# Performance work log

Hardware: AMD Instinct MI355X
Metric: run time of the kernel (lower is better)

Reference implementation:

```python
import jax, jax.numpy as jnp
import numpy as np

NUM_HEADS = 16


def setup_inputs() -> dict:
    key = jax.random.key(0)
    ks = jax.random.split(key, 4)
    B, C, T, D = 1, 1, 3072, 1024
    s = 1.0 / np.sqrt(D)
    return {
        "x": jax.random.normal(ks[0], (B, C, T, D), dtype=jnp.float32),
        "Wq": jax.random.normal(ks[1], (D, D), dtype=jnp.float32) * s,
        "bq": jnp.zeros((D,), dtype=jnp.float32),
        "Wk": jax.random.normal(ks[2], (D, D), dtype=jnp.float32) * s,
        "bk": jnp.zeros((D,), dtype=jnp.float32),
        "Wv": jax.random.normal(ks[3], (D, D), dtype=jnp.float32) * s,
        "bv": jnp.zeros((D,), dtype=jnp.float32),
        "gamma": jnp.float32(0.5),  # learned scalar; 0.0 at torch init, nonzero here for a meaningful signal
    }


def reference(x, Wq, bq, Wk, bk, Wv, bv, gamma):
    # x: (B, C, T, D); Linear acts on last dim (torch: y = x @ W.T + b)
    B, C, T, D = x.shape
    H = NUM_HEADS
    q = (jnp.einsum("bctd,ed->bcte", x, Wq) + bq).reshape(B, -1, T, H)  # (B, X, T, H), X = C*D/H
    k = (jnp.einsum("bctd,ed->bcte", x, Wk) + bk).reshape(B, -1, T, H)
    v = (jnp.einsum("bctd,ed->bcte", x, Wv) + bv).reshape(B, -1, T, H)
    q = q.transpose(0, 3, 2, 1)  # (B, H, T, X)
    k = k.transpose(0, 3, 1, 2)  # (B, H, X, T)
    energy = q @ k               # (B, H, T, T)  -- note: NO 1/sqrt(d) scaling, as in source
    attn = jax.nn.softmax(energy, axis=-1)
    v = v.transpose(0, 3, 2, 1)  # (B, H, T, X)
    out = attn @ v               # (B, H, T, X)
    out = out.transpose(0, 2, 3, 1).reshape(B, T, -1)  # (B, T, X*H) = (B, T, C*D)
    # residual broadcast: (B, T, C*D) + (B, C, T, D); valid since B == C == 1
    return gamma * out + x
```

## Files before the change

### kernel.cpp

```cpp
#include <hip/hip_runtime.h>


typedef _Float16 v8h __attribute__((ext_vector_type(8)));
typedef _Float16 v4h __attribute__((ext_vector_type(4)));
typedef __fp16   v2pk __attribute__((ext_vector_type(2)));
typedef __fp16   v4pk __attribute__((ext_vector_type(4)));
typedef float    v4f __attribute__((ext_vector_type(4)));

#define TSEQ 3072
#define DM   1024
#define NH   16
#define XD   64
#define LOG2E 1.44269504f

__device__ __forceinline__ void async_load16(const void* g, void* l) {
  __builtin_amdgcn_global_load_lds(
      (const __attribute__((address_space(1))) unsigned int*)g,
      (__attribute__((address_space(3))) unsigned int*)l,
      16, 0, 0);
}

__device__ __forceinline__ float fexp2(float x) {
  float r; asm("v_exp_f32 %0, %1" : "=v"(r) : "v"(x)); return r;
}
__device__ __forceinline__ float flog2(float x) {
  float r; asm("v_log_f32 %0, %1" : "=v"(r) : "v"(x)); return r;
}

extern "C" __global__ __launch_bounds__(256) void cvt_kernel(
    const float* __restrict__ x, const float* __restrict__ wq,
    const float* __restrict__ wk, const float* __restrict__ wv,
    _Float16* __restrict__ xb, _Float16* __restrict__ wb)
{
  const int NX4 = (TSEQ * DM) / 4;
  const int NT  = NX4 * 2;
  for (int i = blockIdx.x * blockDim.x + threadIdx.x; i < NT;
       i += gridDim.x * blockDim.x) {
    float4 v;
    _Float16* dst;
    if (i < NX4) {
      v = ((const float4*)x)[i];
      dst = xb + (size_t)i * 4;
    } else {
      const int j = i - NX4;
      const int n = j >> 8;
      if (n < 1024)      v = ((const float4*)wq)[j];
      else if (n < 2048) v = ((const float4*)wk)[j - 262144];
      else               v = ((const float4*)wv)[j - 524288];
      dst = wb + (size_t)j * 4;
    }
    v4h h;
    h[0] = (_Float16)v.x; h[1] = (_Float16)v.y;
    h[2] = (_Float16)v.z; h[3] = (_Float16)v.w;
    *(v4h*)dst = h;
  }
}

extern "C" __global__ __launch_bounds__(256) void qkv_gemm_kernel(
    const _Float16* __restrict__ xb, const _Float16* __restrict__ wb,
    const float* __restrict__ bq, const float* __restrict__ bk,
    const float* __restrict__ bv,
    _Float16* __restrict__ qlin, _Float16* __restrict__ klin,
    _Float16* __restrict__ vlin)
{
  __shared__ _Float16 As[128 * 32];
  __shared__ _Float16 Bs[128 * 32];
  const int tid = threadIdx.x;
  const int w = tid >> 6, l = tid & 63;
  const int li = l & 15, lg = l >> 4;
  const int wm = w >> 1, wn = w & 1;
  const int bid = blockIdx.x;
  const int swz = (bid & 7) * 72 + (bid >> 3);
  const int m0 = (swz / 24) * 128, n0 = (swz % 24) * 128;
  v4f acc[4][4] = {};
  const int srow = l >> 2;
  const int scol = (l & 3) * 8;
  for (int k0 = 0; k0 < DM; k0 += 32) {
#pragma unroll
    for (int c = 0; c < 2; ++c) {
      const int rbase = c * 64 + w * 16;
      async_load16(xb + (size_t)(m0 + rbase + srow) * DM + k0 + scol, &As[rbase * 32]);
      async_load16(wb + (size_t)(n0 + rbase + srow) * DM + k0 + scol, &Bs[rbase * 32]);
    }
    __syncthreads();
    v8h af[4], bf[4];
#pragma unroll
    for (int mi = 0; mi < 4; ++mi)
      af[mi] = *(const v8h*)&As[(wm * 64 + mi * 16 + li) * 32 + lg * 8];
#pragma unroll
    for (int ni = 0; ni < 4; ++ni)
      bf[ni] = *(const v8h*)&Bs[(wn * 64 + ni * 16 + li) * 32 + lg * 8];
#pragma unroll
    for (int mi = 0; mi < 4; ++mi)
#pragma unroll
      for (int ni = 0; ni < 4; ++ni)
        acc[mi][ni] = __builtin_amdgcn_mfma_f32_16x16x32_f16(
            af[mi], bf[ni], acc[mi][ni], 0, 0, 0);
    __syncthreads();
  }
  const int which = n0 >> 10;
  const int ebase = n0 & 1023;
  const float* bias = which == 0 ? bq : (which == 1 ? bk : bv);
  _Float16* outp = which == 0 ? qlin : (which == 1 ? klin : vlin);
#pragma unroll
  for (int mi = 0; mi < 4; ++mi)
#pragma unroll
    for (int r = 0; r < 4; ++r) {
      const int t = m0 + wm * 64 + mi * 16 + lg * 4 + r;
#pragma unroll
      for (int ni = 0; ni < 4; ++ni) {
        const int e = ebase + wn * 64 + ni * 16 + li;
        outp[(size_t)t * DM + e] = (_Float16)(acc[mi][ni][r] + bias[e]);
      }
    }
}

extern "C" __global__ __launch_bounds__(256) void repack_kernel(
    const _Float16* __restrict__ qlin, const _Float16* __restrict__ klin,
    const _Float16* __restrict__ vlin,
    _Float16* __restrict__ qh, _Float16* __restrict__ kh,
    _Float16* __restrict__ vt)
{
  const int NE = NH * TSEQ * XD;
  for (int g = blockIdx.x * blockDim.x + threadIdx.x; g < 3 * NE;
       g += gridDim.x * blockDim.x) {
    if (g < 2 * NE) {
      const int gg = (g < NE) ? g : g - NE;
      const int xx = gg & 63;
      const int rest = gg >> 6;
      const int h = rest / TSEQ;
      const int i = rest - h * TSEQ;
      const int t = xx * 48 + (i >> 6);
      const int e = ((i & 63) << 4) + h;
      if (g < NE) qh[gg] = qlin[t * DM + e];
      else        kh[gg] = (_Float16)((float)klin[t * DM + e] * LOG2E);
    } else {
      const int o = g - 2 * NE;
      const int j = o % TSEQ;
      const int rest = o / TSEQ;
      const int xx = rest & 63;
      const int h = rest >> 6;
      const int t = xx * 48 + (j >> 6);
      const int e = ((j & 63) << 4) + h;
      vt[o] = vlin[t * DM + e];
    }
  }
}

extern "C" __global__ __launch_bounds__(512, 2) void attn_kernel(
    const _Float16* __restrict__ qh, const _Float16* __restrict__ kh,
    const _Float16* __restrict__ vt, _Float16* __restrict__ pOut)
{
  __shared__ _Float16 SH[16384];
  __shared__ float sml[192];
  const int tid = threadIdx.x;
  const int w = tid >> 6, l = tid & 63;
  const int li = l & 15, lg = l >> 4;
  const int rw = w & 3, g = w >> 2;
  const int b = blockIdx.x;
  const int idx = b >> 3;
  const int head = (b & 7) + ((idx >= 16) ? 8 : 0);
  const int i0 = (idx & 15) * 192;
  const size_t hb = (size_t)head * TSEQ * XD;

  v8h qf[3][2];
#pragma unroll
  for (int ct = 0; ct < 3; ++ct) {
    const _Float16* qrow = qh + hb + (size_t)(i0 + rw * 48 + ct * 16 + li) * XD;
    qf[ct][0] = *(const v8h*)(qrow + lg * 8);
    qf[ct][1] = *(const v8h*)(qrow + 32 + lg * 8);
  }
  float m2[3] = {24.0f * LOG2E, 24.0f * LOG2E, 24.0f * LOG2E};
  float l4[3] = {0.0f, 0.0f, 0.0f};
  v4f oacc[4][3] = {};
  const int r8 = l >> 3, c8 = l & 7;

  for (int j0 = 0; j0 < TSEQ; j0 += 128) {
    const int jt = j0 + g * 64;
#pragma unroll
    for (int s = 0; s < 2; ++s) {
      const int n = rw * 2 + s;
      const int row = n * 8 + r8;
      async_load16(kh + hb + (size_t)(jt + row) * XD + ((c8 ^ (row & 7)) * 8),
                   &SH[g * 4096 + n * 512]);
      async_load16(vt + hb + (size_t)row * TSEQ + jt + ((c8 ^ (row & 7)) * 8),
                   &SH[8192 + g * 4096 + n * 512]);
    }
    __syncthreads();
    const _Float16* Kc = &SH[g * 4096];
    const _Float16* Vc = &SH[8192 + g * 4096];

    v4f e4[3][4];
#pragma unroll
    for (int kt = 0; kt < 4; ++kt) {
      const int krow = kt * 16 + li;
      const v8h kf0 = *(const v8h*)&Kc[krow * 64 + ((lg ^ (li & 7)) * 8)];
      const v8h kf1 = *(const v8h*)&Kc[krow * 64 + (((4 + lg) ^ (li & 7)) * 8)];
#pragma unroll
      for (int ct = 0; ct < 3; ++ct) {
        v4f a = {-m2[ct], -m2[ct], -m2[ct], -m2[ct]};
        a = __builtin_amdgcn_mfma_f32_16x16x32_f16(kf0, qf[ct][0], a, 0, 0, 0);
        a = __builtin_amdgcn_mfma_f32_16x16x32_f16(kf1, qf[ct][1], a, 0, 0, 0);
        e4[ct][kt] = a;
      }
    }

    float gm = -1.0e30f;
#pragma unroll
    for (int ct = 0; ct < 3; ++ct)
#pragma unroll
      for (int kt = 0; kt < 4; ++kt)
        gm = fmaxf(fmaxf(gm, fmaxf(e4[ct][kt][0], e4[ct][kt][1])),
                   fmaxf(e4[ct][kt][2], e4[ct][kt][3]));
    if (__any(gm > 11.5f)) {
#pragma unroll
      for (int ct = 0; ct < 3; ++ct) {
        float rm = -1.0e30f;
#pragma unroll
        for (int kt = 0; kt < 4; ++kt)
          rm = fmaxf(fmaxf(rm, fmaxf(e4[ct][kt][0], e4[ct][kt][1])),
                     fmaxf(e4[ct][kt][2], e4[ct][kt][3]));
        rm = fmaxf(rm, __shfl_xor(rm, 16, 64));
        rm = fmaxf(rm, __shfl_xor(rm, 32, 64));
        rm = fmaxf(rm, 0.0f);
        const float fs = fexp2(-rm);
#pragma unroll
        for (int kt = 0; kt < 4; ++kt)
#pragma unroll
          for (int r = 0; r < 4; ++r) e4[ct][kt][r] -= rm;
        l4[ct] *= fs;
#pragma unroll
        for (int mi = 0; mi < 4; ++mi) oacc[mi][ct] *= fs;
        m2[ct] += rm;
      }
    }

    v4h pv[3][4];
#pragma unroll
    for (int ct = 0; ct < 3; ++ct) {
#pragma unroll
      for (int kt = 0; kt < 4; ++kt) {
        const float p0 = fexp2(e4[ct][kt][0]);
        const float p1 = fexp2(e4[ct][kt][1]);
        const float p2 = fexp2(e4[ct][kt][2]);
        const float p3 = fexp2(e4[ct][kt][3]);
        const v2pk lo = __builtin_amdgcn_cvt_pkrtz(p0, p1);
        const v2pk hi = __builtin_amdgcn_cvt_pkrtz(p2, p3);
        const v4pk pk = __builtin_shufflevector(lo, hi, 0, 1, 2, 3);
        pv[ct][kt] = __builtin_bit_cast(v4h, pk);
        l4[ct] += (p0 + p1) + (p2 + p3);
      }
    }

#pragma unroll
    for (int mi = 0; mi < 4; ++mi) {
      const int vrow = mi * 16 + li;
      const int vb = vrow * 64 + (lg & 1) * 4;
#pragma unroll
      for (int kt = 0; kt < 4; ++kt) {
        const v4h vf = *(const v4h*)&Vc[vb + (((kt * 2 + (lg >> 1)) ^ (li & 7)) * 8)];
#pragma unroll
        for (int ct = 0; ct < 3; ++ct)
          oacc[mi][ct] = __builtin_amdgcn_mfma_f32_16x16x16f16(
              vf, pv[ct][kt], oacc[mi][ct], 0, 0, 0);
      }
    }
    __syncthreads();
  }

  float sv[3], inv[3];
#pragma unroll
  for (int ct = 0; ct < 3; ++ct) {
    float ls = l4[ct];
    ls += __shfl_xor(ls, 16, 64);
    ls += __shfl_xor(ls, 32, 64);
    inv[ct] = 1.0f / ls;
    sv[ct] = m2[ct] + flog2(ls);
  }
  _Float16* mb = &SH[0];
  if (g == 1) {
#pragma unroll
    for (int ct = 0; ct < 3; ++ct) {
      const int rl = rw * 48 + ct * 16 + li;
      if (lg == 0) sml[rl] = sv[ct];
#pragma unroll
      for (int mi = 0; mi < 4; ++mi) {
        v4h o4;
#pragma unroll
        for (int r = 0; r < 4; ++r) o4[r] = (_Float16)(oacc[mi][ct][r] * inv[ct]);
        *(v4h*)&mb[rl * 64 + mi * 16 + lg * 4] = o4;
      }
    }
  }
  __syncthreads();
  if (g == 0) {
#pragma unroll
    for (int ct = 0; ct < 3; ++ct) {
      const int rl = rw * 48 + ct * 16 + li;
      const float s1 = sml[rl];
      const float M = fmaxf(sv[ct], s1);
      const float u0 = fexp2(sv[ct] - M), u1 = fexp2(s1 - M);
      const float den = 1.0f / (u0 + u1);
      const float c0 = u0 * den * inv[ct], c1 = u1 * den;
#pragma unroll
      for (int mi = 0; mi < 4; ++mi) {
        const v4h o1 = *(const v4h*)&mb[rl * 64 + mi * 16 + lg * 4];
        v4h o4;
#pragma unroll
        for (int r = 0; r < 4; ++r)
          o4[r] = (_Float16)(c0 * oacc[mi][ct][r] + c1 * (float)o1[r]);
        *(v4h*)&pOut[(size_t)(i0 + rl) * DM + head * 64 + mi * 16 + lg * 4] = o4;
      }
    }
  }
}

extern "C" __global__ __launch_bounds__(256) void epilogue_kernel(
    const _Float16* __restrict__ pO, const float* __restrict__ xin,
    const float* __restrict__ gscal, float* __restrict__ outp)
{
  __shared__ _Float16 po[8 * 1024];
  const int tid = threadIdx.x;
  const size_t t0 = (size_t)blockIdx.x * 8;
  {
    const _Float16* src = pO + t0 * DM + tid * 32;
    v8h* d = (v8h*)&po[tid * 32];
#pragma unroll
    for (int c = 0; c < 4; ++c) d[c] = *(const v8h*)(src + c * 8);
  }
  __syncthreads();
  const float g = gscal[0];
  const int tr = tid >> 5;
  const int d0 = (tid & 31) * 32;
  const size_t rb = (t0 + tr) * DM + d0;
#pragma unroll
  for (int c4 = 0; c4 < 8; ++c4) {
    const float4 xi = *(const float4*)&xin[rb + c4 * 4];
    float4 r;
    r.x = g * (float)po[tr * 1024 + ((c4 * 4 + 0) & 15) * 64 + ((d0 + c4 * 4 + 0) >> 4)] + xi.x;
    r.y = g * (float)po[tr * 1024 + ((c4 * 4 + 1) & 15) * 64 + ((d0 + c4 * 4 + 1) >> 4)] + xi.y;
    r.z = g * (float)po[tr * 1024 + ((c4 * 4 + 2) & 15) * 64 + ((d0 + c4 * 4 + 2) >> 4)] + xi.z;
    r.w = g * (float)po[tr * 1024 + ((c4 * 4 + 3) & 15) * 64 + ((d0 + c4 * 4 + 3) >> 4)] + xi.w;
    *(float4*)&outp[rb + c4 * 4] = r;
  }
}

extern "C" void kernel_launch(void* const* d_in, const int* in_sizes, int n_in,
                              void* d_out, int out_size, void* d_ws, size_t ws_size,
                              hipStream_t stream)
{
  const float* x  = (const float*)d_in[0];
  const float* Wq = (const float*)d_in[1];
  const float* bq = (const float*)d_in[2];
  const float* Wk = (const float*)d_in[3];
  const float* bk = (const float*)d_in[4];
  const float* Wv = (const float*)d_in[5];
  const float* bv = (const float*)d_in[6];
  const float* gm = (const float*)d_in[7];
  float* outp = (float*)d_out;
  char* ws = (char*)d_ws;
  const size_t SZH = (size_t)TSEQ * DM * sizeof(_Float16);
  _Float16* xb   = (_Float16*)(ws);
  _Float16* wb   = (_Float16*)(ws + SZH);
  _Float16* qlin = (_Float16*)(ws + 2 * SZH);
  _Float16* klin = (_Float16*)(ws + 3 * SZH);
  _Float16* vlin = (_Float16*)(ws + 4 * SZH);
  _Float16* qhp  = (_Float16*)(ws + 5 * SZH);
  _Float16* khp  = (_Float16*)(ws + 6 * SZH);
  _Float16* vtp  = (_Float16*)(ws + 7 * SZH);
  _Float16* pO   = (_Float16*)(ws);

  cvt_kernel<<<dim3(1024), dim3(256), 0, stream>>>(x, Wq, Wk, Wv, xb, wb);
  qkv_gemm_kernel<<<dim3(576), dim3(256), 0, stream>>>(xb, wb, bq, bk, bv,
                                                       qlin, klin, vlin);
  repack_kernel<<<dim3(4096), dim3(256), 0, stream>>>(qlin, klin, vlin,
                                                      qhp, khp, vtp);
  attn_kernel<<<dim3(256), dim3(512), 0, stream>>>(qhp, khp, vtp, pO);
  epilogue_kernel<<<dim3(384), dim3(256), 0, stream>>>(pO, x, gm, outp);
  (void)in_sizes; (void)n_in; (void)out_size; (void)ws_size;
}
```

Before: 135.4 us.

## Double-buffer K/V tiles in LDS with async prefetch and MFMA priority hints

Doubles the shared-memory K/V staging area so the next 128-column tile is fetched with global_load_lds while the current tile is being computed. Explicit vmcnt waits and raw s_barrier calls replace __syncthreads, so the load latency overlaps the QK and PV MFMA phases. s_setprio is raised around the MFMA sections so those waves get issue priority. LDS use per block roughly doubles to about 64KB, which could limit residency at two blocks per CU, and the hand-counted vmcnt value must match the number of outstanding loads.

```diff
diff --git a/kernel.cpp b/kernel.cpp
--- a/kernel.cpp
+++ b/kernel.cpp
@@ -147,11 +147,13 @@
   }
 }
 
+#define KOFF(buf, gg) (((buf) * 2 + (gg)) * 4096)
+#define VOFF(buf, gg) (16384 + ((buf) * 2 + (gg)) * 4096)
 extern "C" __global__ __launch_bounds__(512, 2) void attn_kernel(
     const _Float16* __restrict__ qh, const _Float16* __restrict__ kh,
     const _Float16* __restrict__ vt, _Float16* __restrict__ pOut)
 {
-  __shared__ _Float16 SH[16384];
+  __shared__ _Float16 SH[32768];
   __shared__ float sml[192];
   const int tid = threadIdx.x;
   const int w = tid >> 6, l = tid & 63;
@@ -175,22 +177,36 @@
   v4f oacc[4][3] = {};
   const int r8 = l >> 3, c8 = l & 7;
 
-  for (int j0 = 0; j0 < TSEQ; j0 += 128) {
-    const int jt = j0 + g * 64;
+  auto stage = [&](int buf, int jt) {
 #pragma unroll
     for (int s = 0; s < 2; ++s) {
       const int n = rw * 2 + s;
       const int row = n * 8 + r8;
       async_load16(kh + hb + (size_t)(jt + row) * XD + ((c8 ^ (row & 7)) * 8),
-                   &SH[g * 4096 + n * 512]);
+                   &SH[KOFF(buf, g) + n * 512]);
       async_load16(vt + hb + (size_t)row * TSEQ + jt + ((c8 ^ (row & 7)) * 8),
-                   &SH[8192 + g * 4096 + n * 512]);
-    }
-    __syncthreads();
-    const _Float16* Kc = &SH[g * 4096];
-    const _Float16* Vc = &SH[8192 + g * 4096];
+                   &SH[VOFF(buf, g) + n * 512]);
+    }
+  };
+
+  const int NT = TSEQ / 128;
+  stage(0, g * 64);
+  for (int it = 0; it < NT; ++it) {
+    const int cur = it & 1;
+    if (it + 1 < NT) {
+      stage(cur ^ 1, (it + 1) * 128 + g * 64);
+      asm volatile("s_waitcnt vmcnt(4)" ::: "memory");
+    } else {
+      asm volatile("s_waitcnt vmcnt(0)" ::: "memory");
+    }
+    __builtin_amdgcn_sched_barrier(0);
+    __builtin_amdgcn_s_barrier();
+
+    const _Float16* Kc = &SH[KOFF(cur, g)];
+    const _Float16* Vc = &SH[VOFF(cur, g)];
 
     v4f e4[3][4];
+    __builtin_amdgcn_s_setprio(1);
 #pragma unroll
     for (int kt = 0; kt < 4; ++kt) {
       const int krow = kt * 16 + li;
@@ -204,6 +220,7 @@
         e4[ct][kt] = a;
       }
     }
+    __builtin_amdgcn_s_setprio(0);
 
     float gm = -1.0e30f;
 #pragma unroll
@@ -252,6 +269,7 @@
       }
     }
 
+    __builtin_amdgcn_s_setprio(1);
 #pragma unroll
     for (int mi = 0; mi < 4; ++mi) {
       const int vrow = mi * 16 + li;
@@ -265,7 +283,9 @@
               vf, pv[ct][kt], oacc[mi][ct], 0, 0, 0);
       }
     }
-    __syncthreads();
+    __builtin_amdgcn_s_setprio(0);
+    __builtin_amdgcn_sched_barrier(0);
+    __builtin_amdgcn_s_barrier();
   }
 
   float sv[3], inv[3];
```

Result: slower. 138.8 us (+2.5%).

## Load K/V fragments directly from global memory instead of LDS staging

Applied to the files above, without the earlier changes.

Replaces the async global-to-LDS staging of K and V tiles with direct per-wave global loads into MFMA fragments, and removes both per-iteration block barriers. The aim is to cut LDS round-trips and synchronization stalls. In exchange, each K/V tile is fetched separately by the four row-waves that share it, relying on L1/L2 caching, and the V loads become narrow strided accesses. LDS shrinks to the output-merge buffer, which may allow more occupancy.

```diff
diff --git a/kernel.cpp b/kernel.cpp
--- a/kernel.cpp
+++ b/kernel.cpp
@@ -151,7 +151,7 @@
     const _Float16* __restrict__ qh, const _Float16* __restrict__ kh,
     const _Float16* __restrict__ vt, _Float16* __restrict__ pOut)
 {
-  __shared__ _Float16 SH[16384];
+  __shared__ _Float16 mb[192 * 64];
   __shared__ float sml[192];
   const int tid = threadIdx.x;
   const int w = tid >> 6, l = tid & 63;
@@ -173,29 +173,19 @@
   float m2[3] = {24.0f * LOG2E, 24.0f * LOG2E, 24.0f * LOG2E};
   float l4[3] = {0.0f, 0.0f, 0.0f};
   v4f oacc[4][3] = {};
-  const int r8 = l >> 3, c8 = l & 7;
+
+  const _Float16* Kh = kh + hb;
+  const _Float16* Vh = vt + hb;
 
   for (int j0 = 0; j0 < TSEQ; j0 += 128) {
     const int jt = j0 + g * 64;
-#pragma unroll
-    for (int s = 0; s < 2; ++s) {
-      const int n = rw * 2 + s;
-      const int row = n * 8 + r8;
-      async_load16(kh + hb + (size_t)(jt + row) * XD + ((c8 ^ (row & 7)) * 8),
-                   &SH[g * 4096 + n * 512]);
-      async_load16(vt + hb + (size_t)row * TSEQ + jt + ((c8 ^ (row & 7)) * 8),
-                   &SH[8192 + g * 4096 + n * 512]);
-    }
-    __syncthreads();
-    const _Float16* Kc = &SH[g * 4096];
-    const _Float16* Vc = &SH[8192 + g * 4096];
 
     v4f e4[3][4];
 #pragma unroll
     for (int kt = 0; kt < 4; ++kt) {
-      const int krow = kt * 16 + li;
-      const v8h kf0 = *(const v8h*)&Kc[krow * 64 + ((lg ^ (li & 7)) * 8)];
-      const v8h kf1 = *(const v8h*)&Kc[krow * 64 + (((4 + lg) ^ (li & 7)) * 8)];
+      const _Float16* krow = Kh + (size_t)(jt + kt * 16 + li) * XD;
+      const v8h kf0 = *(const v8h*)(krow + lg * 8);
+      const v8h kf1 = *(const v8h*)(krow + 32 + lg * 8);
 #pragma unroll
       for (int ct = 0; ct < 3; ++ct) {
         v4f a = {-m2[ct], -m2[ct], -m2[ct], -m2[ct]};
@@ -254,18 +244,16 @@
 
 #pragma unroll
     for (int mi = 0; mi < 4; ++mi) {
-      const int vrow = mi * 16 + li;
-      const int vb = vrow * 64 + (lg & 1) * 4;
+      const _Float16* vrow = Vh + (size_t)(mi * 16 + li) * TSEQ + jt + lg * 4;
 #pragma unroll
       for (int kt = 0; kt < 4; ++kt) {
-        const v4h vf = *(const v4h*)&Vc[vb + (((kt * 2 + (lg >> 1)) ^ (li & 7)) * 8)];
+        const v4h vf = *(const v4h*)(vrow + kt * 16);
 #pragma unroll
         for (int ct = 0; ct < 3; ++ct)
           oacc[mi][ct] = __builtin_amdgcn_mfma_f32_16x16x16f16(
               vf, pv[ct][kt], oacc[mi][ct], 0, 0, 0);
       }
     }
-    __syncthreads();
   }
 
   float sv[3], inv[3];
@@ -277,7 +265,6 @@
     inv[ct] = 1.0f / ls;
     sv[ct] = m2[ct] + flog2(ls);
   }
-  _Float16* mb = &SH[0];
   if (g == 1) {
 #pragma unroll
     for (int ct = 0; ct < 3; ++ct) {
```

Result: slower. 210.0 us (+55.0%).

## Split attention key range across blocks and merge partials in epilogue

Applied to the files above, without the earlier changes.

Instead of splitting each block's key range between two warp groups and merging in shared memory, each block now handles 384 query rows with all 8 warps over half of the key sequence. The two halves' normalized partial outputs and log-sum-exp values go to global workspace and are combined in the epilogue kernel. This halves per-block LDS use and doubles query rows per block, sharing each K/V tile load across more queries. In exchange it adds extra global writes and reads of two fp16 partial outputs plus LSE arrays.

```diff
diff --git a/kernel.cpp b/kernel.cpp
--- a/kernel.cpp
+++ b/kernel.cpp
@@ -149,24 +149,28 @@
 
 extern "C" __global__ __launch_bounds__(512, 2) void attn_kernel(
     const _Float16* __restrict__ qh, const _Float16* __restrict__ kh,
-    const _Float16* __restrict__ vt, _Float16* __restrict__ pOut)
-{
-  __shared__ _Float16 SH[16384];
-  __shared__ float sml[192];
+    const _Float16* __restrict__ vt,
+    _Float16* __restrict__ oP0, _Float16* __restrict__ oP1,
+    float* __restrict__ sml0, float* __restrict__ sml1)
+{
+  __shared__ _Float16 SH[8192];
   const int tid = threadIdx.x;
   const int w = tid >> 6, l = tid & 63;
   const int li = l & 15, lg = l >> 4;
-  const int rw = w & 3, g = w >> 2;
   const int b = blockIdx.x;
-  const int idx = b >> 3;
-  const int head = (b & 7) + ((idx >= 16) ? 8 : 0);
-  const int i0 = (idx & 15) * 192;
+  const int r = b >> 3;
+  const int head = (b & 7) + 8 * (r & 1);
+  const int qt = (r >> 1) & 7;
+  const int jh = r >> 4;
+  const int i0 = qt * 384;
   const size_t hb = (size_t)head * TSEQ * XD;
+  _Float16* oPart = jh ? oP1 : oP0;
+  float* smlp = jh ? sml1 : sml0;
 
   v8h qf[3][2];
 #pragma unroll
   for (int ct = 0; ct < 3; ++ct) {
-    const _Float16* qrow = qh + hb + (size_t)(i0 + rw * 48 + ct * 16 + li) * XD;
+    const _Float16* qrow = qh + hb + (size_t)(i0 + w * 48 + ct * 16 + li) * XD;
     qf[ct][0] = *(const v8h*)(qrow + lg * 8);
     qf[ct][1] = *(const v8h*)(qrow + 32 + lg * 8);
   }
@@ -174,21 +178,19 @@
   float l4[3] = {0.0f, 0.0f, 0.0f};
   v4f oacc[4][3] = {};
   const int r8 = l >> 3, c8 = l & 7;
-
-  for (int j0 = 0; j0 < TSEQ; j0 += 128) {
-    const int jt = j0 + g * 64;
-#pragma unroll
-    for (int s = 0; s < 2; ++s) {
-      const int n = rw * 2 + s;
-      const int row = n * 8 + r8;
-      async_load16(kh + hb + (size_t)(jt + row) * XD + ((c8 ^ (row & 7)) * 8),
-                   &SH[g * 4096 + n * 512]);
-      async_load16(vt + hb + (size_t)row * TSEQ + jt + ((c8 ^ (row & 7)) * 8),
-                   &SH[8192 + g * 4096 + n * 512]);
+  const int jbase = jh * 1536;
+
+  for (int j0 = jbase; j0 < jbase + 1536; j0 += 64) {
+    {
+      const int row = w * 8 + r8;
+      async_load16(kh + hb + (size_t)(j0 + row) * XD + ((c8 ^ (row & 7)) * 8),
+                   &SH[w * 512]);
+      async_load16(vt + hb + (size_t)row * TSEQ + j0 + ((c8 ^ (row & 7)) * 8),
+                   &SH[4096 + w * 512]);
     }
     __syncthreads();
-    const _Float16* Kc = &SH[g * 4096];
-    const _Float16* Vc = &SH[8192 + g * 4096];
+    const _Float16* Kc = &SH[0];
+    const _Float16* Vc = &SH[4096];
 
     v4f e4[3][4];
 #pragma unroll
@@ -227,7 +229,7 @@
 #pragma unroll
         for (int kt = 0; kt < 4; ++kt)
 #pragma unroll
-          for (int r = 0; r < 4; ++r) e4[ct][kt][r] -= rm;
+          for (int rr = 0; rr < 4; ++rr) e4[ct][kt][rr] -= rm;
         l4[ct] *= fs;
 #pragma unroll
         for (int mi = 0; mi < 4; ++mi) oacc[mi][ct] *= fs;
@@ -268,65 +270,53 @@
     __syncthreads();
   }
 
-  float sv[3], inv[3];
 #pragma unroll
   for (int ct = 0; ct < 3; ++ct) {
     float ls = l4[ct];
     ls += __shfl_xor(ls, 16, 64);
     ls += __shfl_xor(ls, 32, 64);
-    inv[ct] = 1.0f / ls;
-    sv[ct] = m2[ct] + flog2(ls);
-  }
-  _Float16* mb = &SH[0];
-  if (g == 1) {
-#pragma unroll
-    for (int ct = 0; ct < 3; ++ct) {
-      const int rl = rw * 48 + ct * 16 + li;
-      if (lg == 0) sml[rl] = sv[ct];
-#pragma unroll
-      for (int mi = 0; mi < 4; ++mi) {
-        v4h o4;
-#pragma unroll
-        for (int r = 0; r < 4; ++r) o4[r] = (_Float16)(oacc[mi][ct][r] * inv[ct]);
-        *(v4h*)&mb[rl * 64 + mi * 16 + lg * 4] = o4;
-      }
-    }
-  }
-  __syncthreads();
-  if (g == 0) {
-#pragma unroll
-    for (int ct = 0; ct < 3; ++ct) {
-      const int rl = rw * 48 + ct * 16 + li;
-      const float s1 = sml[rl];
-      const float M = fmaxf(sv[ct], s1);
-      const float u0 = fexp2(sv[ct] - M), u1 = fexp2(s1 - M);
-      const float den = 1.0f / (u0 + u1);
-      const float c0 = u0 * den * inv[ct], c1 = u1 * den;
-#pragma unroll
-      for (int mi = 0; mi < 4; ++mi) {
-        const v4h o1 = *(const v4h*)&mb[rl * 64 + mi * 16 + lg * 4];
-        v4h o4;
-#pragma unroll
-        for (int r = 0; r < 4; ++r)
-          o4[r] = (_Float16)(c0 * oacc[mi][ct][r] + c1 * (float)o1[r]);
-        *(v4h*)&pOut[(size_t)(i0 + rl) * DM + head * 64 + mi * 16 + lg * 4] = o4;
-      }
+    const float inv = 1.0f / ls;
+    const int rl = w * 48 + ct * 16 + li;
+    if (lg == 0) smlp[(size_t)(i0 + rl) * NH + head] = m2[ct] + flog2(ls);
+#pragma unroll
+    for (int mi = 0; mi < 4; ++mi) {
+      v4h o4;
+#pragma unroll
+      for (int rr = 0; rr < 4; ++rr) o4[rr] = (_Float16)(oacc[mi][ct][rr] * inv);
+      *(v4h*)&oPart[(size_t)(i0 + rl) * DM + head * 64 + mi * 16 + lg * 4] = o4;
     }
   }
 }
 
 extern "C" __global__ __launch_bounds__(256) void epilogue_kernel(
-    const _Float16* __restrict__ pO, const float* __restrict__ xin,
-    const float* __restrict__ gscal, float* __restrict__ outp)
-{
-  __shared__ _Float16 po[8 * 1024];
+    const _Float16* __restrict__ oP0, const _Float16* __restrict__ oP1,
+    const float* __restrict__ sml0, const float* __restrict__ sml1,
+    const float* __restrict__ xin, const float* __restrict__ gscal,
+    float* __restrict__ outp)
+{
+  __shared__ float po[8 * 1024];
   const int tid = threadIdx.x;
   const size_t t0 = (size_t)blockIdx.x * 8;
   {
-    const _Float16* src = pO + t0 * DM + tid * 32;
-    v8h* d = (v8h*)&po[tid * 32];
-#pragma unroll
-    for (int c = 0; c < 4; ++c) d[c] = *(const v8h*)(src + c * 8);
+    const int tr = tid >> 5;
+    const int c0 = (tid & 31) * 32;
+    const int h = c0 >> 6;
+    const size_t t = t0 + tr;
+    const float s0 = sml0[t * NH + h], s1 = sml1[t * NH + h];
+    const float M = fmaxf(s0, s1);
+    float u0 = fexp2(s0 - M), u1 = fexp2(s1 - M);
+    const float dn = 1.0f / (u0 + u1);
+    u0 *= dn; u1 *= dn;
+    const _Float16* p0 = oP0 + t * DM + c0;
+    const _Float16* p1 = oP1 + t * DM + c0;
+#pragma unroll
+    for (int c = 0; c < 4; ++c) {
+      const v8h a = *(const v8h*)(p0 + c * 8);
+      const v8h bb = *(const v8h*)(p1 + c * 8);
+#pragma unroll
+      for (int e = 0; e < 8; ++e)
+        po[tr * 1024 + c0 + c * 8 + e] = u0 * (float)a[e] + u1 * (float)bb[e];
+    }
   }
   __syncthreads();
   const float g = gscal[0];
@@ -336,12 +326,12 @@
 #pragma unroll
   for (int c4 = 0; c4 < 8; ++c4) {
     const float4 xi = *(const float4*)&xin[rb + c4 * 4];
-    float4 r;
-    r.x = g * (float)po[tr * 1024 + ((c4 * 4 + 0) & 15) * 64 + ((d0 + c4 * 4 + 0) >> 4)] + xi.x;
-    r.y = g * (float)po[tr * 1024 + ((c4 * 4 + 1) & 15) * 64 + ((d0 + c4 * 4 + 1) >> 4)] + xi.y;
-    r.z = g * (float)po[tr * 1024 + ((c4 * 4 + 2) & 15) * 64 + ((d0 + c4 * 4 + 2) >> 4)] + xi.z;
-    r.w = g * (float)po[tr * 1024 + ((c4 * 4 + 3) & 15) * 64 + ((d0 + c4 * 4 + 3) >> 4)] + xi.w;
-    *(float4*)&outp[rb + c4 * 4] = r;
+    float4 rr;
+    rr.x = g * po[tr * 1024 + ((c4 * 4 + 0) & 15) * 64 + ((d0 + c4 * 4 + 0) >> 4)] + xi.x;
+    rr.y = g * po[tr * 1024 + ((c4 * 4 + 1) & 15) * 64 + ((d0 + c4 * 4 + 1) >> 4)] + xi.y;
+    rr.z = g * po[tr * 1024 + ((c4 * 4 + 2) & 15) * 64 + ((d0 + c4 * 4 + 2) >> 4)] + xi.z;
+    rr.w = g * po[tr * 1024 + ((c4 * 4 + 3) & 15) * 64 + ((d0 + c4 * 4 + 3) >> 4)] + xi.w;
+    *(float4*)&outp[rb + c4 * 4] = rr;
   }
 }
 
@@ -368,14 +358,19 @@
   _Float16* qhp  = (_Float16*)(ws + 5 * SZH);
   _Float16* khp  = (_Float16*)(ws + 6 * SZH);
   _Float16* vtp  = (_Float16*)(ws + 7 * SZH);
-  _Float16* pO   = (_Float16*)(ws);
+  _Float16* oP0  = (_Float16*)(ws);
+  _Float16* oP1  = (_Float16*)(ws + SZH);
+  float*    sml0 = (float*)(ws + 3 * SZH);
+  float*    sml1 = sml0 + (size_t)TSEQ * NH;
 
   cvt_kernel<<<dim3(1024), dim3(256), 0, stream>>>(x, Wq, Wk, Wv, xb, wb);
   qkv_gemm_kernel<<<dim3(576), dim3(256), 0, stream>>>(xb, wb, bq, bk, bv,
                                                        qlin, klin, vlin);
   repack_kernel<<<dim3(4096), dim3(256), 0, stream>>>(qlin, klin, vlin,
                                                       qhp, khp, vtp);
-  attn_kernel<<<dim3(256), dim3(512), 0, stream>>>(qhp, khp, vtp, pO);
-  epilogue_kernel<<<dim3(384), dim3(256), 0, stream>>>(pO, x, gm, outp);
+  attn_kernel<<<dim3(256), dim3(512), 0, stream>>>(qhp, khp, vtp,
+                                                   oP0, oP1, sml0, sml1);
+  epilogue_kernel<<<dim3(384), dim3(256), 0, stream>>>(oP0, oP1, sml0, sml1,
+                                                       x, gm, outp);
   (void)in_sizes; (void)n_in; (void)out_size; (void)ws_size;
 }
```

New measurement: 137.7 us. No clear change (+1.7%).
